# Kernel optimization log

Measured on AMD Instinct MI355X. Metric: run time of the kernel, lower is better.

Reference implementation:

```python
import math
import jax, jax.numpy as jnp
import numpy as np

B, C_IN, C_OUT, K, STYLE, H, W = 16, 512, 512, 3, 512, 64, 64


def setup_inputs() -> dict:
    key = jax.random.key(0)
    k1, k2, k3, k4 = jax.random.split(key, 4)
    return {
        "x": jax.random.normal(k1, (B, C_IN, H, W), jnp.float32),
        "style": jax.random.normal(k2, (B, STYLE), jnp.float32),
        "weight": jax.random.normal(k3, (C_OUT, C_IN, K, K), jnp.float32),  # learned conv weight (leading 1 dim of torch param squeezed)
        "mod_w": jax.random.normal(k4, (C_IN, STYLE), jnp.float32),         # EqualLinear weight
        "mod_b": jnp.ones((C_IN,), jnp.float32),                             # EqualLinear bias (bias_init=1)
    }


def reference(x, style, weight, mod_w, mod_b):
    # EqualLinear modulation: scale = 1/sqrt(style_dim), lr_mul = 1
    mod_scale = 1.0 / math.sqrt(STYLE)
    s = style @ (mod_w.T * mod_scale) + mod_b            # [B, C_IN]

    # per-sample modulated weight
    w_scale = 1.0 / math.sqrt(C_IN * K * K)
    w = w_scale * weight[None] * s[:, None, :, None, None]  # [B, C_OUT, C_IN, K, K]

    # demodulate
    demod = jax.lax.rsqrt(jnp.sum(w * w, axis=(2, 3, 4)) + 1e-8)  # [B, C_OUT]
    w = w * demod[:, :, None, None, None]

    pad = K // 2

    def conv_one(xi, wi):
        # xi: [C_IN, H, W], wi: [C_OUT, C_IN, K, K]
        return jax.lax.conv_general_dilated(
            xi[None], wi, window_strides=(1, 1),
            padding=[(pad, pad), (pad, pad)],
            dimension_numbers=("NCHW", "OIHW", "NCHW"),
        )[0]

    return jax.vmap(conv_one)(x, w)  # [B, C_OUT, H, W]
```

## Files before the change

### kernel.cpp

```cpp
#include <hip/hip_runtime.h>
#include <hip/hip_bf16.h>
#include <math.h>
#include <stdint.h>

#define B_     16
#define CI_    512
#define CO_    512
#define HH     64
#define WW     64
#define STYLE_ 512

typedef __bf16 bf16x8 __attribute__((ext_vector_type(8)));
typedef float f32x4 __attribute__((ext_vector_type(4)));

#define WS_S     0
#define WS_DEMOD 32768
#define WS_WSQ   65536
#define WS_WB    1114112
#define WS_XS    5832704

__device__ __forceinline__ void gload16(const void* g, void* l) {
    __builtin_amdgcn_global_load_lds((const __attribute__((address_space(1))) uint32_t*)g,
                                     (__attribute__((address_space(3))) uint32_t*)l, 16, 0, 0);
}

__global__ void k_style(const float* __restrict__ style, const float* __restrict__ mod_w,
                        const float* __restrict__ mod_b, float* __restrict__ s_out) {
    int b  = blockIdx.x;
    int ci = threadIdx.x;
    const float scale = 0.044194173824159216f;
    float acc = 0.f;
    const float* st = style + b * STYLE_;
    const float* mw = mod_w + (size_t)ci * STYLE_;
    for (int j = 0; j < STYLE_; ++j) acc += st[j] * mw[j];
    s_out[b * CI_ + ci] = acc * scale + mod_b[ci];
}

__global__ void k_wsq(const float* __restrict__ weight, float* __restrict__ wsq) {
    int p = blockIdx.x * blockDim.x + threadIdx.x;
    int co = p >> 9, ci = p & 511;
    const float* wp = weight + (size_t)p * 9;
    float acc = 0.f;
    for (int t = 0; t < 9; ++t) { float v = wp[t]; acc += v * v; }
    wsq[(size_t)ci * CO_ + co] = acc;
}

__global__ void k_demod(const float* __restrict__ s, const float* __restrict__ wsq,
                        float* __restrict__ demod) {
    int b = blockIdx.x, co = threadIdx.x;
    const float w_scale2 = 1.0f / 4608.0f;
    float acc = 0.f;
    const float* sb = s + b * CI_;
    for (int ci = 0; ci < CI_; ++ci) { float sv = sb[ci]; acc += sv * sv * wsq[(size_t)ci * CO_ + co]; }
    demod[b * CO_ + co] = 1.0f / sqrtf(acc * w_scale2 + 1e-8f);
}

__global__ __launch_bounds__(256) void k_wb(const float* __restrict__ weight, __bf16* __restrict__ wb) {
    int p = blockIdx.x * 256 + threadIdx.x;
    int co = p >> 9, ci = p & 511;
    const float* wp = weight + (size_t)p * 9;
    #pragma unroll
    for (int t = 0; t < 9; ++t)
        wb[((((size_t)(ci >> 5) * 9 + t) * CO_) + co) * 32 + (ci & 31)] = (__bf16)wp[t];
}

__global__ __launch_bounds__(256) void k_guard(uint32_t* __restrict__ xs32) {
    int i = blockIdx.x * 256 + threadIdx.x;
    int dw = i & 1023, row2 = (i >> 10) & 1, b = (i >> 11) & 15, chunk = i >> 15;
    xs32[(((size_t)chunk * 16 + b) * 66 + row2 * 65) * 1024 + dw] = 0;
}

__global__ __launch_bounds__(256) void k_xs(const float* __restrict__ x, const float* __restrict__ s,
                                            __bf16* __restrict__ xs) {
    __shared__ float Lt[64][65];
    const int y = blockIdx.x, b = blockIdx.y;
    const int tid = threadIdx.x;
    const float w_scale = 0.014731391274719739f;
    for (int ci0 = 0; ci0 < CI_; ci0 += 64) {
        for (int i = tid; i < 64 * 64; i += 256) {
            int ci = i >> 6, xx = i & 63;
            Lt[ci][xx] = x[((size_t)(b * CI_ + ci0 + ci) * HH + y) * WW + xx]
                         * s[b * CI_ + ci0 + ci] * w_scale;
        }
        __syncthreads();
        for (int o = tid; o < 512; o += 256) {
            int xx = o >> 3, oct = o & 7;
            int cb = ci0 + oct * 8;
            bf16x8 v;
            #pragma unroll
            for (int j = 0; j < 8; ++j) v[j] = (__bf16)Lt[oct * 8 + j][xx];
            size_t idx = ((((size_t)(cb >> 5) * 16 + b) * 66 + (y + 1)) * 64 + xx) * 32 + (cb & 31);
            *(bf16x8*)&xs[idx] = v;
        }
        __syncthreads();
    }
}

#define XB 42240
#define WB 36864

__global__ __launch_bounds__(512, 1) void k_conv(
    const __bf16* __restrict__ xs, const __bf16* __restrict__ wb,
    const float* __restrict__ demod, float* __restrict__ out)
{
    __shared__ __align__(128) char smem[2 * XB + 2 * WB];

    const int tid  = threadIdx.x;
    const int lane = tid & 63;
    const int wave = tid >> 6;

    const int bid  = blockIdx.x;
    const int r8   = bid & 7;
    const int q    = bid >> 3;
    const int co0  = (q & 7) * 64;
    const int pair = (q >> 3) | (r8 << 4);
    const int y0   = (pair & 7) * 8;
    const int b    = pair >> 3;

    const int m  = lane & 15;
    const int g  = lane >> 4;
    const int qA = g ^ ((m >> 1) & 3);

    for (int i = tid; i < 640; i += 512) {
        int dw = i & 15, h = i >> 4;
        int buf = h / 20, hh = h % 20;
        int rr = hh >> 1, side = hh & 1;
        ((uint32_t*)smem)[buf * (XB / 4) + (rr * 66 + side * 65) * 16 + dw] = 0;
    }
    asm volatile("s_waitcnt lgkmcnt(0)" ::: "memory");

    f32x4 acc[4][4];
    #pragma unroll
    for (int mi = 0; mi < 4; ++mi)
        #pragma unroll
        for (int nt = 0; nt < 4; ++nt) acc[mi][nt] = (f32x4){0.f, 0.f, 0.f, 0.f};

    auto stage = [&](int chunk, int sel) {
        if (wave < 4) {
            const __bf16* xsc = xs + ((size_t)chunk * 16 + b) * (66 * 64 * 32);
            #pragma unroll
            for (int i = 0; i < 10; ++i) {
                int o = wave * 10 + i;
                int r = o >> 2, seg = o & 3;
                int p = seg * 64 + lane;
                int xr = 1 + (p >> 2), qd = p & 3;
                int rowg = r * 66 + xr;
                int sq = qd ^ ((rowg >> 1) & 3);
                const __bf16* src = xsc + ((size_t)((y0 + r) * 64 + (xr - 1))) * 32 + sq * 8;
                gload16(src, smem + sel * XB + (r * 66 + 1) * 64 + seg * 1024);
            }
        } else {
            const __bf16* wbc = wb + (size_t)chunk * 9 * CO_ * 32;
            #pragma unroll
            for (int i = 0; i < 9; ++i) {
                int j = (wave - 4) * 9 + i;
                int p = j * 64 + lane;
                int row = p >> 2, qd = p & 3;
                int sq = qd ^ ((row >> 1) & 3);
                const __bf16* src = wbc + ((size_t)((row >> 6) * CO_ + co0 + (row & 63))) * 32 + sq * 8;
                gload16(src, smem + 2 * XB + sel * WB + j * 1024);
            }
        }
    };

    stage(0, 0);

    for (int t = 0; t < 16; ++t) {
        if (t < 15) {
            stage(t + 1, (t + 1) & 1);
            if (wave < 4) asm volatile("s_waitcnt vmcnt(10)" ::: "memory");
            else          asm volatile("s_waitcnt vmcnt(9)"  ::: "memory");
        } else {
            asm volatile("s_waitcnt vmcnt(0)" ::: "memory");
        }
        __builtin_amdgcn_s_barrier();

        const __bf16* ldsX = (const __bf16*)(smem + (t & 1) * XB);
        const __bf16* ldsW = (const __bf16*)(smem + 2 * XB + (t & 1) * WB);

        #pragma unroll
        for (int kh = 0; kh < 3; ++kh) {
            #pragma unroll
            for (int kw = 0; kw < 3; ++kw) {
                const int tp = kh * 3 + kw;
                bf16x8 a0 = *(const bf16x8*)&ldsW[(tp * 64 +  0 + m) * 32 + qA * 8];
                bf16x8 a1 = *(const bf16x8*)&ldsW[(tp * 64 + 16 + m) * 32 + qA * 8];
                bf16x8 a2 = *(const bf16x8*)&ldsW[(tp * 64 + 32 + m) * 32 + qA * 8];
                bf16x8 a3 = *(const bf16x8*)&ldsW[(tp * 64 + 48 + m) * 32 + qA * 8];
                #pragma unroll
                for (int nt = 0; nt < 4; ++nt) {
                    const int rowg = (wave + kh) * 66 + nt * 16 + m + kw;
                    const int qB = g ^ ((rowg >> 1) & 3);
                    bf16x8 bv = *(const bf16x8*)&ldsX[rowg * 32 + qB * 8];
                    acc[0][nt] = __builtin_amdgcn_mfma_f32_16x16x32_bf16(a0, bv, acc[0][nt], 0, 0, 0);
                    acc[1][nt] = __builtin_amdgcn_mfma_f32_16x16x32_bf16(a1, bv, acc[1][nt], 0, 0, 0);
                    acc[2][nt] = __builtin_amdgcn_mfma_f32_16x16x32_bf16(a2, bv, acc[2][nt], 0, 0, 0);
                    acc[3][nt] = __builtin_amdgcn_mfma_f32_16x16x32_bf16(a3, bv, acc[3][nt], 0, 0, 0);
                }
            }
        }
        __builtin_amdgcn_s_barrier();
    }

    const int y = y0 + wave;
    #pragma unroll
    for (int mi = 0; mi < 4; ++mi) {
        #pragma unroll
        for (int j = 0; j < 4; ++j) {
            const int co = co0 + mi * 16 + g * 4 + j;
            const float dm = demod[b * CO_ + co];
            float* op = out + ((size_t)(b * CO_ + co) * HH + y) * WW;
            #pragma unroll
            for (int nt = 0; nt < 4; ++nt)
                op[nt * 16 + m] = acc[mi][nt][j] * dm;
        }
    }
}

extern "C" void kernel_launch(void* const* d_in, const int* in_sizes, int n_in,
                              void* d_out, int out_size, void* d_ws, size_t ws_size,
                              hipStream_t stream) {
    const float* x      = (const float*)d_in[0];
    const float* style  = (const float*)d_in[1];
    const float* weight = (const float*)d_in[2];
    const float* mod_w  = (const float*)d_in[3];
    const float* mod_b  = (const float*)d_in[4];
    float* out = (float*)d_out;

    char* wsb = (char*)d_ws;
    float*  s_buf = (float*)(wsb + WS_S);
    float*  demod = (float*)(wsb + WS_DEMOD);
    float*  wsq   = (float*)(wsb + WS_WSQ);
    __bf16* wb    = (__bf16*)(wsb + WS_WB);
    __bf16* xs    = (__bf16*)(wsb + WS_XS);

    k_style<<<dim3(B_), dim3(CI_), 0, stream>>>(style, mod_w, mod_b, s_buf);
    k_wsq<<<dim3(CO_ * CI_ / 512), dim3(512), 0, stream>>>(weight, wsq);
    k_demod<<<dim3(B_), dim3(CO_), 0, stream>>>(s_buf, wsq, demod);
    k_wb<<<dim3(CO_ * CI_ / 256), dim3(256), 0, stream>>>(weight, wb);
    k_guard<<<dim3(2048), dim3(256), 0, stream>>>((uint32_t*)xs);
    k_xs<<<dim3(HH, B_), dim3(256), 0, stream>>>(x, s_buf, xs);
    k_conv<<<dim3(1024), dim3(512), 0, stream>>>(xs, wb, demod, out);
}
```

Measured before the change: 341.1 us.

## Fuse weight prep kernels, fold guard zeroing into xs, restructure conv inner loop

Merges the weight-square and bf16 weight repack kernels into one pass, and moves the guard-row zeroing into the activation scaling kernel, so two kernel launches go away. The activation kernel now reads x with float4 loads. The conv kernel precomputes its staging and LDS addresses once, preloads all 36 weight fragments per chunk before the MFMA loop, raises wave priority around the MFMAs, and asks for two blocks per CU. Holding those fragments raises register pressure, and with about 158KB of LDS per block a second block likely cannot fit anyway.

Measured after the change: 365.7 us. +7.2%, slower.

```diff
diff --git a/kernel.cpp b/kernel.cpp
--- a/kernel.cpp
+++ b/kernel.cpp
@@ -36,12 +36,18 @@
     s_out[b * CI_ + ci] = acc * scale + mod_b[ci];
 }
 
-__global__ void k_wsq(const float* __restrict__ weight, float* __restrict__ wsq) {
-    int p = blockIdx.x * blockDim.x + threadIdx.x;
+__global__ __launch_bounds__(256) void k_wprep(const float* __restrict__ weight,
+                                               float* __restrict__ wsq, __bf16* __restrict__ wb) {
+    int p = blockIdx.x * 256 + threadIdx.x;
     int co = p >> 9, ci = p & 511;
     const float* wp = weight + (size_t)p * 9;
     float acc = 0.f;
-    for (int t = 0; t < 9; ++t) { float v = wp[t]; acc += v * v; }
+    #pragma unroll
+    for (int t = 0; t < 9; ++t) {
+        float v = wp[t];
+        acc += v * v;
+        wb[((((size_t)(ci >> 5) * 9 + t) * CO_) + co) * 32 + (ci & 31)] = (__bf16)v;
+    }
     wsq[(size_t)ci * CO_ + co] = acc;
 }
 
@@ -55,21 +61,6 @@
     demod[b * CO_ + co] = 1.0f / sqrtf(acc * w_scale2 + 1e-8f);
 }
 
-__global__ __launch_bounds__(256) void k_wb(const float* __restrict__ weight, __bf16* __restrict__ wb) {
-    int p = blockIdx.x * 256 + threadIdx.x;
-    int co = p >> 9, ci = p & 511;
-    const float* wp = weight + (size_t)p * 9;
-    #pragma unroll
-    for (int t = 0; t < 9; ++t)
-        wb[((((size_t)(ci >> 5) * 9 + t) * CO_) + co) * 32 + (ci & 31)] = (__bf16)wp[t];
-}
-
-__global__ __launch_bounds__(256) void k_guard(uint32_t* __restrict__ xs32) {
-    int i = blockIdx.x * 256 + threadIdx.x;
-    int dw = i & 1023, row2 = (i >> 10) & 1, b = (i >> 11) & 15, chunk = i >> 15;
-    xs32[(((size_t)chunk * 16 + b) * 66 + row2 * 65) * 1024 + dw] = 0;
-}
-
 __global__ __launch_bounds__(256) void k_xs(const float* __restrict__ x, const float* __restrict__ s,
                                             __bf16* __restrict__ xs) {
     __shared__ float Lt[64][65];
@@ -77,10 +68,14 @@
     const int tid = threadIdx.x;
     const float w_scale = 0.014731391274719739f;
     for (int ci0 = 0; ci0 < CI_; ci0 += 64) {
-        for (int i = tid; i < 64 * 64; i += 256) {
-            int ci = i >> 6, xx = i & 63;
-            Lt[ci][xx] = x[((size_t)(b * CI_ + ci0 + ci) * HH + y) * WW + xx]
-                         * s[b * CI_ + ci0 + ci] * w_scale;
+        for (int i = tid; i < 64 * 16; i += 256) {
+            int ci = i >> 4, x4 = (i & 15) * 4;
+            const float4 v = *(const float4*)&x[((size_t)(b * CI_ + ci0 + ci) * HH + y) * WW + x4];
+            float sc = s[b * CI_ + ci0 + ci] * w_scale;
+            Lt[ci][x4]     = v.x * sc;
+            Lt[ci][x4 + 1] = v.y * sc;
+            Lt[ci][x4 + 2] = v.z * sc;
+            Lt[ci][x4 + 3] = v.w * sc;
         }
         __syncthreads();
         for (int o = tid; o < 512; o += 256) {
@@ -94,12 +89,19 @@
         }
         __syncthreads();
     }
+    if (y == 0 || y == 63) {
+        const int row = (y == 0) ? 0 : 65;
+        uint32_t* xs32 = (uint32_t*)xs;
+        for (int c = 0; c < 16; ++c)
+            for (int i = tid; i < 1024; i += 256)
+                xs32[(((size_t)c * 16 + b) * 66 + row) * 1024 + i] = 0;
+    }
 }
 
 #define XB 42240
 #define WB 36864
 
-__global__ __launch_bounds__(512, 1) void k_conv(
+__global__ __launch_bounds__(512, 2) void k_conv(
     const __bf16* __restrict__ xs, const __bf16* __restrict__ wb,
     const float* __restrict__ demod, float* __restrict__ out)
 {
@@ -129,45 +131,75 @@
     }
     asm volatile("s_waitcnt lgkmcnt(0)" ::: "memory");
 
+    uint32_t soff[10];
+    uint32_t sdst[10];
+    const __bf16* sb;
+    size_t sstride;
+    uint32_t selstride;
+    if (wave < 4) {
+        sb = xs + (size_t)b * (66 * 64 * 32);
+        sstride = (size_t)16 * 66 * 64 * 32;
+        selstride = XB;
+        #pragma unroll
+        for (int i = 0; i < 10; ++i) {
+            int o = wave * 10 + i, r = o >> 2, seg = o & 3;
+            int p = seg * 64 + lane;
+            int xr = 1 + (p >> 2), qd = p & 3;
+            int rowg = r * 66 + xr;
+            int sq = qd ^ ((rowg >> 1) & 3);
+            soff[i] = (uint32_t)(((y0 + r) * 64 + (xr - 1)) * 32 + sq * 8);
+            sdst[i] = (uint32_t)((r * 66 + 1) * 64 + seg * 1024);
+        }
+    } else {
+        sb = wb;
+        sstride = (size_t)9 * CO_ * 32;
+        selstride = WB;
+        #pragma unroll
+        for (int i = 0; i < 9; ++i) {
+            int j = (wave - 4) * 9 + i;
+            int p = j * 64 + lane;
+            int row = p >> 2, qd = p & 3;
+            int sq = qd ^ ((row >> 1) & 3);
+            soff[i] = (uint32_t)(((row >> 6) * CO_ + co0 + (row & 63)) * 32 + sq * 8);
+            sdst[i] = (uint32_t)(2 * XB + j * 1024);
+        }
+        soff[9] = 0; sdst[9] = 2 * XB;
+    }
+
+    uint32_t bbase[9];
+    #pragma unroll
+    for (int kh = 0; kh < 3; ++kh)
+        #pragma unroll
+        for (int kw = 0; kw < 3; ++kw) {
+            int R = (wave + kh) * 66 + m + kw;
+            int qB = g ^ ((R >> 1) & 3);
+            bbase[kh * 3 + kw] = (uint32_t)(R * 64 + qB * 16);
+        }
+    const uint32_t abase = (uint32_t)(m * 64 + qA * 16);
+
     f32x4 acc[4][4];
     #pragma unroll
     for (int mi = 0; mi < 4; ++mi)
         #pragma unroll
         for (int nt = 0; nt < 4; ++nt) acc[mi][nt] = (f32x4){0.f, 0.f, 0.f, 0.f};
 
-    auto stage = [&](int chunk, int sel) {
+    auto stage = [&](const __bf16* base, int sel) {
+        uint32_t so = sel * selstride;
         if (wave < 4) {
-            const __bf16* xsc = xs + ((size_t)chunk * 16 + b) * (66 * 64 * 32);
-            #pragma unroll
-            for (int i = 0; i < 10; ++i) {
-                int o = wave * 10 + i;
-                int r = o >> 2, seg = o & 3;
-                int p = seg * 64 + lane;
-                int xr = 1 + (p >> 2), qd = p & 3;
-                int rowg = r * 66 + xr;
-                int sq = qd ^ ((rowg >> 1) & 3);
-                const __bf16* src = xsc + ((size_t)((y0 + r) * 64 + (xr - 1))) * 32 + sq * 8;
-                gload16(src, smem + sel * XB + (r * 66 + 1) * 64 + seg * 1024);
-            }
+            #pragma unroll
+            for (int i = 0; i < 10; ++i) gload16(base + soff[i], smem + so + sdst[i]);
         } else {
-            const __bf16* wbc = wb + (size_t)chunk * 9 * CO_ * 32;
-            #pragma unroll
-            for (int i = 0; i < 9; ++i) {
-                int j = (wave - 4) * 9 + i;
-                int p = j * 64 + lane;
-                int row = p >> 2, qd = p & 3;
-                int sq = qd ^ ((row >> 1) & 3);
-                const __bf16* src = wbc + ((size_t)((row >> 6) * CO_ + co0 + (row & 63))) * 32 + sq * 8;
-                gload16(src, smem + 2 * XB + sel * WB + j * 1024);
-            }
+            #pragma unroll
+            for (int i = 0; i < 9; ++i) gload16(base + soff[i], smem + so + sdst[i]);
         }
     };
 
-    stage(0, 0);
+    stage(sb, 0);
 
     for (int t = 0; t < 16; ++t) {
         if (t < 15) {
-            stage(t + 1, (t + 1) & 1);
+            sb += sstride;
+            stage(sb, (t + 1) & 1);
             if (wave < 4) asm volatile("s_waitcnt vmcnt(10)" ::: "memory");
             else          asm volatile("s_waitcnt vmcnt(9)"  ::: "memory");
         } else {
@@ -175,30 +207,29 @@
         }
         __builtin_amdgcn_s_barrier();
 
-        const __bf16* ldsX = (const __bf16*)(smem + (t & 1) * XB);
-        const __bf16* ldsW = (const __bf16*)(smem + 2 * XB + (t & 1) * WB);
-
-        #pragma unroll
-        for (int kh = 0; kh < 3; ++kh) {
-            #pragma unroll
-            for (int kw = 0; kw < 3; ++kw) {
-                const int tp = kh * 3 + kw;
-                bf16x8 a0 = *(const bf16x8*)&ldsW[(tp * 64 +  0 + m) * 32 + qA * 8];
-                bf16x8 a1 = *(const bf16x8*)&ldsW[(tp * 64 + 16 + m) * 32 + qA * 8];
-                bf16x8 a2 = *(const bf16x8*)&ldsW[(tp * 64 + 32 + m) * 32 + qA * 8];
-                bf16x8 a3 = *(const bf16x8*)&ldsW[(tp * 64 + 48 + m) * 32 + qA * 8];
-                #pragma unroll
-                for (int nt = 0; nt < 4; ++nt) {
-                    const int rowg = (wave + kh) * 66 + nt * 16 + m + kw;
-                    const int qB = g ^ ((rowg >> 1) & 3);
-                    bf16x8 bv = *(const bf16x8*)&ldsX[rowg * 32 + qB * 8];
-                    acc[0][nt] = __builtin_amdgcn_mfma_f32_16x16x32_bf16(a0, bv, acc[0][nt], 0, 0, 0);
-                    acc[1][nt] = __builtin_amdgcn_mfma_f32_16x16x32_bf16(a1, bv, acc[1][nt], 0, 0, 0);
-                    acc[2][nt] = __builtin_amdgcn_mfma_f32_16x16x32_bf16(a2, bv, acc[2][nt], 0, 0, 0);
-                    acc[3][nt] = __builtin_amdgcn_mfma_f32_16x16x32_bf16(a3, bv, acc[3][nt], 0, 0, 0);
-                }
+        const char* xbuf = smem + (t & 1) * XB;
+        const char* wbuf = smem + 2 * XB + (t & 1) * WB + abase;
+
+        bf16x8 af[9][4];
+        #pragma unroll
+        for (int tp = 0; tp < 9; ++tp)
+            #pragma unroll
+            for (int mi = 0; mi < 4; ++mi)
+                af[tp][mi] = *(const bf16x8*)(wbuf + tp * 4096 + mi * 1024);
+
+        __builtin_amdgcn_s_setprio(1);
+        #pragma unroll
+        for (int tp = 0; tp < 9; ++tp) {
+            #pragma unroll
+            for (int nt = 0; nt < 4; ++nt) {
+                bf16x8 bv = *(const bf16x8*)(xbuf + bbase[tp] + nt * 1024);
+                acc[0][nt] = __builtin_amdgcn_mfma_f32_16x16x32_bf16(af[tp][0], bv, acc[0][nt], 0, 0, 0);
+                acc[1][nt] = __builtin_amdgcn_mfma_f32_16x16x32_bf16(af[tp][1], bv, acc[1][nt], 0, 0, 0);
+                acc[2][nt] = __builtin_amdgcn_mfma_f32_16x16x32_bf16(af[tp][2], bv, acc[2][nt], 0, 0, 0);
+                acc[3][nt] = __builtin_amdgcn_mfma_f32_16x16x32_bf16(af[tp][3], bv, acc[3][nt], 0, 0, 0);
             }
         }
+        __builtin_amdgcn_s_setprio(0);
         __builtin_amdgcn_s_barrier();
     }
 
@@ -235,10 +266,8 @@
     __bf16* xs    = (__bf16*)(wsb + WS_XS);
 
     k_style<<<dim3(B_), dim3(CI_), 0, stream>>>(style, mod_w, mod_b, s_buf);
-    k_wsq<<<dim3(CO_ * CI_ / 512), dim3(512), 0, stream>>>(weight, wsq);
+    k_wprep<<<dim3(CO_ * CI_ / 256), dim3(256), 0, stream>>>(weight, wsq, wb);
     k_demod<<<dim3(B_), dim3(CO_), 0, stream>>>(s_buf, wsq, demod);
-    k_wb<<<dim3(CO_ * CI_ / 256), dim3(256), 0, stream>>>(weight, wb);
-    k_guard<<<dim3(2048), dim3(256), 0, stream>>>((uint32_t*)xs);
     k_xs<<<dim3(HH, B_), dim3(256), 0, stream>>>(x, s_buf, xs);
     k_conv<<<dim3(1024), dim3(512), 0, stream>>>(xs, wb, demod, out);
 }
```
